# Kernel tuning notes

Measured on AMD Instinct MI355X. Metric: run time of the kernel, lower is better.

## Reference

```python
import jax, jax.numpy as jnp
import numpy as np

UNITS, N, S = 256, 64, 4
BATCH, T = 64, 1024


def setup_inputs() -> dict:
    key = jax.random.key(0)
    k0, k1, k2, k3 = jax.random.split(key, 4)
    return {
        "inputs": jax.random.uniform(k0, (BATCH, T, S), dtype=jnp.float32),
        "transition_kernel": jax.random.normal(k1, (UNITS, N, N), dtype=jnp.float32),
        "emission_kernel": jax.random.normal(k2, (UNITS, N, S), dtype=jnp.float32),
        "init_kernel": jax.random.normal(k3, (UNITS, N), dtype=jnp.float32),
    }


def reference(inputs, transition_kernel, emission_kernel, init_kernel):
    # Softmaxed HMM parameters (computed once; the TF cell recomputes per step).
    A = jax.nn.softmax(transition_kernel, axis=-1)  # [U, N, N] transitions
    B = jax.nn.softmax(emission_kernel, axis=-1)    # [U, N, S] emissions
    I = jax.nn.softmax(init_kernel, axis=-1)        # [U, N]    initial dist

    batch = inputs.shape[0]
    U, Nn = init_kernel.shape

    alpha0 = jnp.zeros((batch, U, Nn), dtype=inputs.dtype)
    ll0 = jnp.zeros((batch, U), dtype=inputs.dtype)
    is_init0 = jnp.ones((batch,), dtype=inputs.dtype)  # HMM starts in init at t=0

    def step(carry, x_t):
        alpha, ll, is_init = carry
        # R[b,u,j] = is_init[b]*I[u,j] + sum_i A[u,i,j]*alpha[b,u,i]  (A^T matvec)
        R = is_init[:, None, None] * I[None] + jnp.einsum("uij,bui->buj", A, alpha)
        # E[b,u,i] = sum_c B[u,i,c] * x_t[b,c]
        E = jnp.einsum("unc,bc->bun", B, x_t)
        fwd = E * R                              # [B, U, N]
        Ssum = jnp.sum(fwd, axis=-1)             # [B, U]
        ll = ll + jnp.log(Ssum)
        alpha = fwd / Ssum[..., None]            # normalized forward variable
        return (alpha, ll, jnp.zeros_like(is_init)), ll

    xs = jnp.swapaxes(inputs, 0, 1)  # [T, B, S]
    (_, _, _), lls = jax.lax.scan(step, (alpha0, ll0, is_init0), xs)
    # whole-sequence output: cumulative log-likelihood per step, [B, T, U]
    return jnp.swapaxes(lls, 0, 1)
```

## Files before the change

kernel.cpp:

```cpp
#include <hip/hip_runtime.h>


#define U_ 256
#define N_ 64
#define S_ 4
#define B_ 64
#define T_ 1024
#define ROWP 72

typedef __attribute__((ext_vector_type(8))) __bf16 bf16x8;
typedef __attribute__((ext_vector_type(4))) float floatx4;

__device__ __forceinline__ int sig(int jt, int m) {
    return 32 * (jt >> 1) + 4 * (jt & 1) + 8 * (m >> 2) + (m & 3);
}

__launch_bounds__(256, 1)
__global__ void hmm_fwd_kernel(const float* __restrict__ xg,
                               const float* __restrict__ trans,
                               const float* __restrict__ emis,
                               const float* __restrict__ initk,
                               float* __restrict__ out)
{
    __shared__ __bf16 AT[N_ * ROWP];
    __shared__ float BemS[N_][S_];
    __shared__ float IS[N_];

    const int bid = blockIdx.x;
    const int u = ((bid & 7) << 5) | (bid >> 3);
    const int tid = threadIdx.x;
    const int lane = tid & 63;
    const int w = tid >> 6;
    const int q = lane >> 4;
    const int l = lane & 15;

    if (tid < 64) {
        const float* rowp = trans + (u * N_ + tid) * N_;
        float v[N_];
        #pragma unroll
        for (int k = 0; k < 16; ++k) {
            floatx4 t4 = *(const floatx4*)(rowp + 4 * k);
            v[4*k] = t4.x; v[4*k+1] = t4.y; v[4*k+2] = t4.z; v[4*k+3] = t4.w;
        }
        float m = v[0];
        #pragma unroll
        for (int j = 1; j < N_; ++j) m = fmaxf(m, v[j]);
        float s = 0.f;
        #pragma unroll
        for (int j = 0; j < N_; ++j) { v[j] = __expf(v[j] - m); s += v[j]; }
        float inv = 1.0f / s;
        #pragma unroll
        for (int j = 0; j < N_; ++j) AT[j * ROWP + tid] = (__bf16)(v[j] * inv);
    } else if (tid < 128) {
        int n = tid - 64;
        floatx4 e4 = *(const floatx4*)(emis + (u * N_ + n) * S_);
        float m = fmaxf(fmaxf(e4.x, e4.y), fmaxf(e4.z, e4.w));
        float a = __expf(e4.x - m), b2 = __expf(e4.y - m);
        float c = __expf(e4.z - m), d = __expf(e4.w - m);
        float inv = 1.0f / (a + b2 + c + d);
        BemS[n][0] = a*inv; BemS[n][1] = b2*inv; BemS[n][2] = c*inv; BemS[n][3] = d*inv;
    } else if (tid < 192) {
        int j = tid - 128;
        float v = initk[u * N_ + j];
        float m = v;
        #pragma unroll
        for (int s = 1; s < 64; s <<= 1) m = fmaxf(m, __shfl_xor(m, s, 64));
        float e = __expf(v - m);
        float ssum = e;
        #pragma unroll
        for (int s = 1; s < 64; s <<= 1) ssum += __shfl_xor(ssum, s, 64);
        IS[j] = e / ssum;
    }
    __syncthreads();

    bf16x8 afrag[4][2];
    #pragma unroll
    for (int jt = 0; jt < 4; ++jt)
        #pragma unroll
        for (int kt = 0; kt < 2; ++kt)
            afrag[jt][kt] = *(const bf16x8*)&AT[sig(jt, l) * ROWP + 32*kt + 8*q];

    bf16x8 afragE[4];
    #pragma unroll
    for (int jt = 0; jt < 4; ++jt) {
        #pragma unroll
        for (int p = 0; p < 8; ++p) afragE[jt][p] = (__bf16)0.f;
        if (q == 0) {
            #pragma unroll
            for (int c = 0; c < 4; ++c)
                afragE[jt][c] = (__bf16)BemS[sig(jt, l)][c];
        }
    }

    floatx4 Rv[4];
    #pragma unroll
    for (int jt = 0; jt < 4; ++jt)
        #pragma unroll
        for (int r = 0; r < 4; ++r) Rv[jt][r] = IS[sig(jt, 4*q + r)];

    __asm__ volatile("" ::: "memory");

    const int b = 16*w + l;
    const float* xin = xg + b * (T_ * S_);
    float* llout = out + (size_t)b * T_ * U_ + u;

    const floatx4 z = {0.f, 0.f, 0.f, 0.f};
    floatx4 Ev[4];
    float rsA = 1.0f;

    bf16x8 be;
    #pragma unroll
    for (int p = 0; p < 8; ++p) be[p] = (__bf16)0.f;

    floatx4 x0 = *(const floatx4*)xin;
    floatx4 xvA[4], xvB[4];
    #pragma unroll
    for (int i = 0; i < 4; ++i)
        xvA[i] = *(const floatx4*)(xin + (1 + i) * S_);

    {
        be[0] = (__bf16)x0.x; be[1] = (__bf16)x0.y;
        be[2] = (__bf16)x0.z; be[3] = (__bf16)x0.w;
        #pragma unroll
        for (int jt = 0; jt < 4; ++jt)
            Ev[jt] = __builtin_amdgcn_mfma_f32_16x16x32_bf16(afragE[jt], be, z, 0, 0, 0);
    }

    float hist[8];
    float e1 = 1.0f, pe1 = 1.0f, Cacc = 0.f;
    bool own = false, ownN = false;
    float pp0, pa16, pa32, pa48;

    auto consume = [&](int kprev) {
        float ss = (pp0 + pa16) + (pa32 + pa48);
        rsA = __builtin_amdgcn_rcpf(ss);
        hist[kprev] = own ? ss : hist[kprev];
        if (kprev == 7) e1 = ownN ? ss : e1;
    };

    auto step = [&](const floatx4& xsrc, int slot) {
        floatx4 gv[4];
        #pragma unroll
        for (int jt = 0; jt < 4; ++jt) gv[jt] = Ev[jt] * Rv[jt];

        bf16x8 bf0, bf1;
        #pragma unroll
        for (int p = 0; p < 4; ++p) {
            bf0[p]     = (__bf16)gv[0][p];
            bf0[4 + p] = (__bf16)gv[1][p];
            bf1[p]     = (__bf16)gv[2][p];
            bf1[4 + p] = (__bf16)gv[3][p];
        }

        #pragma unroll
        for (int jt = 0; jt < 4; ++jt) {
            floatx4 acc = __builtin_amdgcn_mfma_f32_16x16x32_bf16(afrag[jt][0], bf0, z, 0, 0, 0);
            Rv[jt] = __builtin_amdgcn_mfma_f32_16x16x32_bf16(afrag[jt][1], bf1, acc, 0, 0, 0);
        }

        if (slot > 0) consume(slot - 1);

        floatx4 xs = xsrc * rsA;
        be[0] = (__bf16)xs.x; be[1] = (__bf16)xs.y;
        be[2] = (__bf16)xs.z; be[3] = (__bf16)xs.w;
        #pragma unroll
        for (int jt = 0; jt < 4; ++jt)
            Ev[jt] = __builtin_amdgcn_mfma_f32_16x16x32_bf16(afragE[jt], be, z, 0, 0, 0);

        floatx4 s4 = (gv[0] + gv[1]) + (gv[2] + gv[3]);
        pp0  = (s4.x + s4.y) + (s4.z + s4.w);
        pa16 = __shfl_xor(pp0, 16, 64);
        pa32 = __shfl_xor(pp0, 32, 64);
        pa48 = __shfl_xor(pp0, 48, 64);
    };

    for (int tb = 0; tb < T_; tb += 8) {
        const int oct = (tb >> 3) & 3;
        own  = (q == oct);
        ownN = (q == ((oct + 1) & 3));
        if ((tb & 24) == 0) pe1 = e1;

        #pragma unroll
        for (int i = 0; i < 4; ++i) {
            int ti = tb + 5 + i; ti = (ti < T_) ? ti : T_ - 1;
            xvB[i] = *(const floatx4*)(xin + ti * S_);
        }

        step(xvA[0], 0); step(xvA[1], 1); step(xvA[2], 2); step(xvA[3], 3);

        #pragma unroll
        for (int i = 0; i < 4; ++i) {
            int ti = tb + 9 + i; ti = (ti < T_) ? ti : T_ - 1;
            xvA[i] = *(const floatx4*)(xin + ti * S_);
        }

        step(xvB[0], 4); step(xvB[1], 5); step(xvB[2], 6); step(xvB[3], 7);

        consume(7);

        if ((tb & 24) == 24) {
            const int tb0 = tb - 24;
            float sg[8], P[8];
            #pragma unroll
            for (int k = 0; k < 8; ++k) sg[k] = __logf(hist[k]);
            P[0] = sg[0];
            #pragma unroll
            for (int k = 1; k < 8; ++k) P[k] = P[k-1] + sg[k];
            float Loc = P[7];
            float a  = __shfl_xor(Loc, 16, 64);
            float b2 = __shfl_xor(Loc, 32, 64);
            float c  = __shfl_xor(Loc, 48, 64);
            float bc = b2 + c;
            float off = ((q & 1) ? a : 0.f) + ((q & 2) ? bc : 0.f);
            float base = Cacc + off;
            float se1 = __logf((q == 0) ? pe1 : e1);
            float* fp = llout + (size_t)(tb0 + 8 * q) * U_;
            fp[0]          = sg[0] + base - se1;
            fp[U_]         = sg[1] + base;
            #pragma unroll
            for (int k = 2; k < 8; ++k)
                fp[(size_t)k * U_] = sg[k] + base + P[k-2];
            Cacc += Loc + a + bc;
        }
    }
}

extern "C" void kernel_launch(void* const* d_in, const int* in_sizes, int n_in,
                              void* d_out, int out_size, void* d_ws, size_t ws_size,
                              hipStream_t stream) {
    const float* xg    = (const float*)d_in[0];
    const float* trans = (const float*)d_in[1];
    const float* emis  = (const float*)d_in[2];
    const float* initk = (const float*)d_in[3];
    float* out = (float*)d_out;
    hipLaunchKernelGGL(hmm_fwd_kernel, dim3(U_), dim3(256), 0, stream,
                       xg, trans, emis, initk, out);
}
```

Measured before the change: 359.8 us.

## Replace per-step reciprocal normalization with power-of-two rescale every eight steps

The per-step division by the running sum (rcp of the reduced sum, then scaling of x before the emission MFMA) is removed from the serial recurrence. Instead the forward variable Rv is rescaled by an exact power of two, taken from the exponent of a sum every 8 steps, and the log-likelihood bookkeeping is rebuilt around these exponent offsets. Inputs are now packed into bf16 fragments at load time and the time loop is unrolled by groups of four. This shortens the dependency chain between consecutive steps. In exchange, unnormalized values drift in magnitude across up to 8 steps, and the log-output reconstruction is more intricate.

```diff
diff --git a/kernel.cpp b/kernel.cpp
--- a/kernel.cpp
+++ b/kernel.cpp
@@ -7,6 +7,7 @@
 #define B_ 64
 #define T_ 1024
 #define ROWP 72
+#define LN2F 0.69314718055994530942f
 
 typedef __attribute__((ext_vector_type(8))) __bf16 bf16x8;
 typedef __attribute__((ext_vector_type(4))) float floatx4;
@@ -106,39 +107,40 @@
 
     const floatx4 z = {0.f, 0.f, 0.f, 0.f};
     floatx4 Ev[4];
-    float rsA = 1.0f;
-
-    bf16x8 be;
-    #pragma unroll
-    for (int p = 0; p < 8; ++p) be[p] = (__bf16)0.f;
-
-    floatx4 x0 = *(const floatx4*)xin;
-    floatx4 xvA[4], xvB[4];
+
+    auto packbe = [&](floatx4 x4) {
+        bf16x8 t;
+        t[0] = (__bf16)x4.x; t[1] = (__bf16)x4.y;
+        t[2] = (__bf16)x4.z; t[3] = (__bf16)x4.w;
+        t[4] = (__bf16)0.f;  t[5] = (__bf16)0.f;
+        t[6] = (__bf16)0.f;  t[7] = (__bf16)0.f;
+        return t;
+    };
+
+    {
+        bf16x8 be0 = packbe(*(const floatx4*)xin);
+        #pragma unroll
+        for (int jt = 0; jt < 4; ++jt)
+            Ev[jt] = __builtin_amdgcn_mfma_f32_16x16x32_bf16(afragE[jt], be0, z, 0, 0, 0);
+    }
+    bf16x8 beA[4], beB[4];
     #pragma unroll
     for (int i = 0; i < 4; ++i)
-        xvA[i] = *(const floatx4*)(xin + (1 + i) * S_);
-
-    {
-        be[0] = (__bf16)x0.x; be[1] = (__bf16)x0.y;
-        be[2] = (__bf16)x0.z; be[3] = (__bf16)x0.w;
-        #pragma unroll
-        for (int jt = 0; jt < 4; ++jt)
-            Ev[jt] = __builtin_amdgcn_mfma_f32_16x16x32_bf16(afragE[jt], be, z, 0, 0, 0);
-    }
+        beA[i] = packbe(*(const floatx4*)(xin + (1 + i) * S_));
 
     float hist[8];
-    float e1 = 1.0f, pe1 = 1.0f, Cacc = 0.f;
-    bool own = false, ownN = false;
-    float pp0, pa16, pa32, pa48;
-
-    auto consume = [&](int kprev) {
+    float ssf = 1.0f;
+    float pp0 = 0.f, pa16 = 0.f, pa32 = 0.f, pa48 = 0.f;
+    float Cacc = 0.f;
+    float kfv[4] = {0.f, 0.f, 0.f, 0.f};
+
+    auto consume = [&](int kprev, bool o) {
         float ss = (pp0 + pa16) + (pa32 + pa48);
-        rsA = __builtin_amdgcn_rcpf(ss);
-        hist[kprev] = own ? ss : hist[kprev];
-        if (kprev == 7) e1 = ownN ? ss : e1;
+        hist[kprev] = o ? ss : hist[kprev];
+        if (kprev == 5) ssf = ss;
     };
 
-    auto step = [&](const floatx4& xsrc, int slot) {
+    auto step = [&](const bf16x8& beS, int slot, bool own, bool ownP) {
         floatx4 gv[4];
         #pragma unroll
         for (int jt = 0; jt < 4; ++jt) gv[jt] = Ev[jt] * Rv[jt];
@@ -158,14 +160,11 @@
             Rv[jt] = __builtin_amdgcn_mfma_f32_16x16x32_bf16(afrag[jt][1], bf1, acc, 0, 0, 0);
         }
 
-        if (slot > 0) consume(slot - 1);
-
-        floatx4 xs = xsrc * rsA;
-        be[0] = (__bf16)xs.x; be[1] = (__bf16)xs.y;
-        be[2] = (__bf16)xs.z; be[3] = (__bf16)xs.w;
+        if (slot == 0) consume(7, ownP); else consume(slot - 1, own);
+
         #pragma unroll
         for (int jt = 0; jt < 4; ++jt)
-            Ev[jt] = __builtin_amdgcn_mfma_f32_16x16x32_bf16(afragE[jt], be, z, 0, 0, 0);
+            Ev[jt] = __builtin_amdgcn_mfma_f32_16x16x32_bf16(afragE[jt], beS, z, 0, 0, 0);
 
         floatx4 s4 = (gv[0] + gv[1]) + (gv[2] + gv[3]);
         pp0  = (s4.x + s4.y) + (s4.z + s4.w);
@@ -174,54 +173,49 @@
         pa48 = __shfl_xor(pp0, 48, 64);
     };
 
-    for (int tb = 0; tb < T_; tb += 8) {
-        const int oct = (tb >> 3) & 3;
-        own  = (q == oct);
-        ownN = (q == ((oct + 1) & 3));
-        if ((tb & 24) == 0) pe1 = e1;
-
-        #pragma unroll
-        for (int i = 0; i < 4; ++i) {
-            int ti = tb + 5 + i; ti = (ti < T_) ? ti : T_ - 1;
-            xvB[i] = *(const floatx4*)(xin + ti * S_);
-        }
-
-        step(xvA[0], 0); step(xvA[1], 1); step(xvA[2], 2); step(xvA[3], 3);
-
-        #pragma unroll
-        for (int i = 0; i < 4; ++i) {
-            int ti = tb + 9 + i; ti = (ti < T_) ? ti : T_ - 1;
-            xvA[i] = *(const floatx4*)(xin + ti * S_);
-        }
-
-        step(xvB[0], 4); step(xvB[1], 5); step(xvB[2], 6); step(xvB[3], 7);
-
-        consume(7);
-
-        if ((tb & 24) == 24) {
-            const int tb0 = tb - 24;
-            float sg[8], P[8];
-            #pragma unroll
-            for (int k = 0; k < 8; ++k) sg[k] = __logf(hist[k]);
-            P[0] = sg[0];
-            #pragma unroll
-            for (int k = 1; k < 8; ++k) P[k] = P[k-1] + sg[k];
-            float Loc = P[7];
-            float a  = __shfl_xor(Loc, 16, 64);
-            float b2 = __shfl_xor(Loc, 32, 64);
-            float c  = __shfl_xor(Loc, 48, 64);
-            float bc = b2 + c;
-            float off = ((q & 1) ? a : 0.f) + ((q & 2) ? bc : 0.f);
-            float base = Cacc + off;
-            float se1 = __logf((q == 0) ? pe1 : e1);
-            float* fp = llout + (size_t)(tb0 + 8 * q) * U_;
-            fp[0]          = sg[0] + base - se1;
-            fp[U_]         = sg[1] + base;
-            #pragma unroll
-            for (int k = 2; k < 8; ++k)
-                fp[(size_t)k * U_] = sg[k] + base + P[k-2];
-            Cacc += Loc + a + bc;
-        }
+    for (int tbb = 0; tbb < T_; tbb += 32) {
+        #pragma unroll
+        for (int g = 0; g < 4; ++g) {
+            const int tb = tbb + 8 * g;
+            const bool own  = (q == g);
+            const bool ownP = (q == ((g + 3) & 3));
+
+            #pragma unroll
+            for (int i = 0; i < 4; ++i) {
+                int ti = tb + 5 + i; ti = (ti < T_) ? ti : T_ - 1;
+                beB[i] = packbe(*(const floatx4*)(xin + ti * S_));
+            }
+
+            step(beA[0], 0, own, ownP); step(beA[1], 1, own, ownP);
+            step(beA[2], 2, own, ownP); step(beA[3], 3, own, ownP);
+
+            #pragma unroll
+            for (int i = 0; i < 4; ++i) {
+                int ti = tb + 9 + i; ti = (ti < T_) ? ti : T_ - 1;
+                beA[i] = packbe(*(const floatx4*)(xin + ti * S_));
+            }
+
+            step(beB[0], 4, own, ownP); step(beB[1], 5, own, ownP);
+            step(beB[2], 6, own, ownP); step(beB[3], 7, own, ownP);
+
+            if (g == 3) consume(7, own);
+
+            unsigned eb = (__float_as_uint(ssf) >> 23) & 255u;
+            float f = __uint_as_float((254u - eb) << 23);
+            #pragma unroll
+            for (int jt = 0; jt < 4; ++jt) Rv[jt] *= f;
+            kfv[g] = (float)((int)eb - 127);
+        }
+
+        float s01  = kfv[0] + kfv[1];
+        float s012 = s01 + kfv[2];
+        float offk = (q == 1) ? kfv[0] : ((q == 2) ? s01 : ((q == 3) ? s012 : 0.f));
+        float base = Cacc + LN2F * offk;
+        float* fp = llout + (size_t)(tbb + 8 * q) * U_;
+        #pragma unroll
+        for (int k = 0; k < 8; ++k)
+            fp[(size_t)k * U_] = __logf(hist[k]) + base;
+        Cacc += LN2F * (s012 + kfv[3]);
     }
 }
 
```

After: 482.5 us. 34.1% more time.
